# Kernel optimization log

Hardware: AMD Instinct MI355X
Metric: run time of the kernel (lower is better)

The kernel has to match this reference:

```python
import jax, jax.numpy as jnp
import numpy as np

G = 8          # num_groups
GIN = 2048 // G   # group_in_features
GOUT = 2048 // G  # group_out_features


def setup_inputs() -> dict:
    key = jax.random.key(0)
    kx, kw, kb = jax.random.split(key, 3)
    x = jax.random.normal(kx, (8192, 2048), dtype=jnp.float32)
    # per-group linear params, torch nn.Linear default init scale ~ U(-1/sqrt(fan_in), ...)
    bound = 1.0 / np.sqrt(GIN)
    W = jax.random.uniform(kw, (G, GIN, GOUT), minval=-bound, maxval=bound, dtype=jnp.float32)
    b = jax.random.uniform(kb, (G, GOUT), minval=-bound, maxval=bound, dtype=jnp.float32)
    # rational activation coeffs, init p=[1,0,0,0], q=[1,0,0] per group
    p = jnp.tile(jnp.array([1.0, 0.0, 0.0, 0.0], dtype=jnp.float32), (G, 1))
    q = jnp.tile(jnp.array([1.0, 0.0, 0.0], dtype=jnp.float32), (G, 1))
    return {"x": x, "W": W, "b": b, "p": p, "q": q}


def _rational(y, p, q):
    # y: [N, G, GOUT]; p: [G, 4]; q: [G, 3] -> broadcast over N and GOUT
    p = p[None, :, :, None]  # [1,G,4,1]
    q = q[None, :, :, None]  # [1,G,3,1]
    y2 = y * y
    y3 = y2 * y
    num = p[:, :, 0] + p[:, :, 1] * y + p[:, :, 2] * y2 + p[:, :, 3] * y3
    den = 1.0 + jnp.abs(q[:, :, 0] * y + q[:, :, 1] * y2 + q[:, :, 2] * y3)
    return num / den


def reference(x, W, b, p, q):
    N = x.shape[0]
    xg = x.reshape(N, G, GIN)                       # chunk along last dim
    y = jnp.einsum('ngi,gio->ngo', xg, W) + b[None]  # grouped GEMM, [N,G,GOUT]
    out = _rational(y, p, q)
    return out.reshape(N, G * GOUT)                 # cat along last dim
```

## Files before the change

kernel.cpp:

```cpp
#include <hip/hip_runtime.h>
#include <hip/hip_bf16.h>

#define G_ 8
#define GIN_ 256
#define GOUT_ 256
#define NROWS_ 8192
#define LDX_ 2048

typedef __attribute__((ext_vector_type(4))) float f32x4;
typedef __attribute__((ext_vector_type(8))) short bf16x8;

__device__ __forceinline__ void lds_barrier() {
    asm volatile("s_waitcnt lgkmcnt(0)\n\ts_barrier" ::: "memory");
}

__global__ __launch_bounds__(256) void wprep_kernel(const float* __restrict__ W,
                                                    __hip_bfloat16* __restrict__ Wt) {
    __shared__ float tile[64][65];
    const int bid = blockIdx.x;
    const int g  = bid >> 4;
    const int ot = (bid >> 2) & 3;
    const int it = bid & 3;
    const float* Wg = W + g * GIN_ * GOUT_;
    __hip_bfloat16* Wtg = Wt + g * GIN_ * GOUT_;
    const int lane_o = threadIdx.x & 63;
    const int sub    = threadIdx.x >> 6;
#pragma unroll
    for (int r = 0; r < 16; ++r) {
        int i = r * 4 + sub;
        tile[i][lane_o] = Wg[(it * 64 + i) * GOUT_ + ot * 64 + lane_o];
    }
    __syncthreads();
#pragma unroll
    for (int r = 0; r < 16; ++r) {
        int o = r * 4 + sub;
        Wtg[(ot * 64 + o) * GIN_ + it * 64 + lane_o] = __float2bfloat16(tile[lane_o][o]);
    }
}

__global__ __launch_bounds__(256, 4) void gkan_kernel(const float* __restrict__ x,
                                                      const __hip_bfloat16* __restrict__ Wt,
                                                      const float* __restrict__ bias,
                                                      const float* __restrict__ pc,
                                                      const float* __restrict__ qc,
                                                      float* __restrict__ out) {
    __shared__ __align__(16) __hip_bfloat16 As[32 * 256];

    const int bid    = blockIdx.x;
    const int g      = bid & 7;
    const int ch     = (bid >> 3) & 1;
    const int mblock = bid >> 4;
    const int row0   = mblock * 32;

    const int t    = threadIdx.x;
    const int wave = t >> 6;
    const int lane = t & 63;
    const int lm   = lane & 15;
    const int quad = lane >> 4;
    const int colbase = ch * 128 + wave * 32;

    const int sr = t >> 3;
    const int su = t & 7;
    const float* xs = x + (size_t)(row0 + sr) * LDX_ + g * GIN_ + su * 32;
    f32x4 st[8];
#pragma unroll
    for (int j = 0; j < 8; ++j)
        st[j] = *(const f32x4*)(xs + j * 4);

    bf16x8 Breg[2][8];
    {
        const __hip_bfloat16* Wg = Wt + (size_t)g * (GIN_ * GOUT_)
                                      + (size_t)colbase * GIN_;
#pragma unroll
        for (int nt = 0; nt < 2; ++nt)
#pragma unroll
            for (int c = 0; c < 8; ++c)
                Breg[nt][c] = *(const bf16x8*)(Wg + (size_t)(nt * 16 + lm) * GIN_
                                                  + c * 32 + quad * 8);
    }

    const float p0 = pc[g * 4 + 0], p1 = pc[g * 4 + 1];
    const float p2 = pc[g * 4 + 2], p3 = pc[g * 4 + 3];
    const float q0 = qc[g * 3 + 0], q1 = qc[g * 3 + 1], q2 = qc[g * 3 + 2];
    float bb[2];
#pragma unroll
    for (int nt = 0; nt < 2; ++nt)
        bb[nt] = bias[g * GOUT_ + colbase + nt * 16 + lm];

    {
        __hip_bfloat16* rowp = &As[sr * 256];
#pragma unroll
        for (int k = 0; k < 4; ++k) {
            union { __hip_bfloat16 h[8]; bf16x8 v; } cv;
            const f32x4 a = st[2 * k], b = st[2 * k + 1];
            cv.h[0] = __float2bfloat16(a.x); cv.h[1] = __float2bfloat16(a.y);
            cv.h[2] = __float2bfloat16(a.z); cv.h[3] = __float2bfloat16(a.w);
            cv.h[4] = __float2bfloat16(b.x); cv.h[5] = __float2bfloat16(b.y);
            cv.h[6] = __float2bfloat16(b.z); cv.h[7] = __float2bfloat16(b.w);
            *(bf16x8*)(rowp + (((4 * su + k) ^ (sr & 7)) * 8)) = cv.v;
        }
    }
    lds_barrier();

    f32x4 acc[2][2] = {};
#pragma unroll
    for (int c = 0; c < 8; ++c) {
        bf16x8 af[2];
#pragma unroll
        for (int mt = 0; mt < 2; ++mt) {
            const int gh = (c * 4 + quad) ^ (lm & 7);
            af[mt] = *(const bf16x8*)(As + (mt * 16 + lm) * 256 + gh * 8);
        }
#pragma unroll
        for (int mt = 0; mt < 2; ++mt)
#pragma unroll
            for (int nt = 0; nt < 2; ++nt)
                acc[mt][nt] = __builtin_amdgcn_mfma_f32_16x16x32_bf16(
                    af[mt], Breg[nt][c], acc[mt][nt], 0, 0, 0);
    }

#pragma unroll
    for (int nt = 0; nt < 2; ++nt) {
        const int col = g * GOUT_ + colbase + nt * 16 + lm;
#pragma unroll
        for (int mt = 0; mt < 2; ++mt)
#pragma unroll
            for (int r = 0; r < 4; ++r) {
                const int row = row0 + mt * 16 + quad * 4 + r;
                const float y   = acc[mt][nt][r] + bb[nt];
                const float num = p0 + y * (p1 + y * (p2 + y * p3));
                const float den = 1.0f + fabsf(y * (q0 + y * (q1 + y * q2)));
                out[(size_t)row * LDX_ + col] = num * __builtin_amdgcn_rcpf(den);
            }
    }
}

extern "C" void kernel_launch(void* const* d_in, const int* in_sizes, int n_in,
                              void* d_out, int out_size, void* d_ws, size_t ws_size,
                              hipStream_t stream) {
    const float* x = (const float*)d_in[0];
    const float* W = (const float*)d_in[1];
    const float* b = (const float*)d_in[2];
    const float* p = (const float*)d_in[3];
    const float* q = (const float*)d_in[4];
    float* out = (float*)d_out;

    __hip_bfloat16* Wt = (__hip_bfloat16*)d_ws;

    wprep_kernel<<<128, 256, 0, stream>>>(W, Wt);
    gkan_kernel<<<4096, 256, 0, stream>>>(x, Wt, b, p, q, out);
}
```

Baseline: 150.8 us.

## Pre-tile weights into MFMA fragment order and widen block to full group

The weight prep kernel now writes bf16 weights directly in MFMA fragment layout, so each lane loads its B fragment with one contiguous 16-byte read per k-step. The main kernel uses 512-thread blocks covering all 256 output columns of a group, which halves the grid and removes the duplicate x-tile load and conversion that two column halves previously did. B fragments are streamed inside a non-unrolled k loop instead of being preloaded into registers, and the A tile uses a new blocked, swizzled LDS layout. This lowers register pressure and x traffic, at the cost of global weight loads sitting on the MFMA critical path with less latency hiding.

Measured after the change: 133.3 us. -11.6%, faster.

```diff
diff --git a/kernel.cpp b/kernel.cpp
--- a/kernel.cpp
+++ b/kernel.cpp
@@ -19,64 +19,97 @@
     __shared__ float tile[64][65];
     const int bid = blockIdx.x;
     const int g  = bid >> 4;
-    const int ot = (bid >> 2) & 3;
-    const int it = bid & 3;
-    const float* Wg = W + g * GIN_ * GOUT_;
-    __hip_bfloat16* Wtg = Wt + g * GIN_ * GOUT_;
+    const int kt = (bid >> 2) & 3;
+    const int ct = bid & 3;
+    const float* Wg = W + g * (GIN_ * GOUT_);
+    __hip_bfloat16* Wo = Wt + (size_t)g * (GIN_ * GOUT_);
     const int lane_o = threadIdx.x & 63;
     const int sub    = threadIdx.x >> 6;
 #pragma unroll
     for (int r = 0; r < 16; ++r) {
         int i = r * 4 + sub;
-        tile[i][lane_o] = Wg[(it * 64 + i) * GOUT_ + ot * 64 + lane_o];
+        tile[i][lane_o] = Wg[(kt * 64 + i) * GOUT_ + ct * 64 + lane_o];
     }
     __syncthreads();
+    const int col = threadIdx.x & 63;
+    const int kgb = threadIdx.x >> 6;
 #pragma unroll
-    for (int r = 0; r < 16; ++r) {
-        int o = r * 4 + sub;
-        Wtg[(ot * 64 + o) * GIN_ + it * 64 + lane_o] = __float2bfloat16(tile[lane_o][o]);
+    for (int h = 0; h < 2; ++h) {
+        const int kg    = kgb + h * 4;
+        const int kglob = kt * 64 + kg * 8;
+        const int c     = kglob >> 5;
+        const int quad  = (kglob >> 3) & 3;
+        const int colg  = ct * 64 + col;
+        const int cb    = colg >> 4;
+        const int c16   = colg & 15;
+        union { __hip_bfloat16 hh[8]; bf16x8 v; } cv;
+#pragma unroll
+        for (int j = 0; j < 8; ++j)
+            cv.hh[j] = __float2bfloat16(tile[kg * 8 + j][col]);
+        *(bf16x8*)(Wo + (size_t)(c * 16 + cb) * 512 + c16 * 32 + quad * 8) = cv.v;
     }
 }
 
-__global__ __launch_bounds__(256, 4) void gkan_kernel(const float* __restrict__ x,
+__global__ __launch_bounds__(512, 8) void gkan_kernel(const float* __restrict__ x,
                                                       const __hip_bfloat16* __restrict__ Wt,
                                                       const float* __restrict__ bias,
                                                       const float* __restrict__ pc,
                                                       const float* __restrict__ qc,
                                                       float* __restrict__ out) {
-    __shared__ __align__(16) __hip_bfloat16 As[32 * 256];
+    __shared__ __align__(16) __hip_bfloat16 As[8192];
 
-    const int bid    = blockIdx.x;
-    const int g      = bid & 7;
-    const int ch     = (bid >> 3) & 1;
-    const int mblock = bid >> 4;
-    const int row0   = mblock * 32;
+    const int bid  = blockIdx.x;
+    const int g    = bid & 7;
+    const int row0 = (bid >> 3) * 32;
 
     const int t    = threadIdx.x;
     const int wave = t >> 6;
     const int lane = t & 63;
     const int lm   = lane & 15;
-    const int quad = lane >> 4;
-    const int colbase = ch * 128 + wave * 32;
+    const int q    = lane >> 4;
 
-    const int sr = t >> 3;
-    const int su = t & 7;
-    const float* xs = x + (size_t)(row0 + sr) * LDX_ + g * GIN_ + su * 32;
-    f32x4 st[8];
-#pragma unroll
-    for (int j = 0; j < 8; ++j)
-        st[j] = *(const f32x4*)(xs + j * 4);
+    const int row = t >> 4;
+    const int su  = t & 15;
+    const float* xs = x + (size_t)(row0 + row) * LDX_ + g * GIN_ + su * 8;
+    f32x4 a0 = *(const f32x4*)(xs);
+    f32x4 a1 = *(const f32x4*)(xs + 4);
+    f32x4 b0 = *(const f32x4*)(xs + 128);
+    f32x4 b1 = *(const f32x4*)(xs + 132);
 
-    bf16x8 Breg[2][8];
     {
-        const __hip_bfloat16* Wg = Wt + (size_t)g * (GIN_ * GOUT_)
-                                      + (size_t)colbase * GIN_;
-#pragma unroll
-        for (int nt = 0; nt < 2; ++nt)
-#pragma unroll
-            for (int c = 0; c < 8; ++c)
-                Breg[nt][c] = *(const bf16x8*)(Wg + (size_t)(nt * 16 + lm) * GIN_
-                                                  + c * 32 + quad * 8);
+        const int rblk = row >> 4, r16 = row & 15, rx = row & 3;
+        const int c0 = su >> 2, quad = su & 3;
+        const int slot = (quad ^ rx) * 8 + r16 * 32;
+        union { __hip_bfloat16 hh[8]; bf16x8 v; } ca, cb;
+        ca.hh[0] = __float2bfloat16(a0.x); ca.hh[1] = __float2bfloat16(a0.y);
+        ca.hh[2] = __float2bfloat16(a0.z); ca.hh[3] = __float2bfloat16(a0.w);
+        ca.hh[4] = __float2bfloat16(a1.x); ca.hh[5] = __float2bfloat16(a1.y);
+        ca.hh[6] = __float2bfloat16(a1.z); ca.hh[7] = __float2bfloat16(a1.w);
+        cb.hh[0] = __float2bfloat16(b0.x); cb.hh[1] = __float2bfloat16(b0.y);
+        cb.hh[2] = __float2bfloat16(b0.z); cb.hh[3] = __float2bfloat16(b0.w);
+        cb.hh[4] = __float2bfloat16(b1.x); cb.hh[5] = __float2bfloat16(b1.y);
+        cb.hh[6] = __float2bfloat16(b1.z); cb.hh[7] = __float2bfloat16(b1.w);
+        *(bf16x8*)(As + (c0 * 2 + rblk) * 512 + slot)       = ca.v;
+        *(bf16x8*)(As + ((4 + c0) * 2 + rblk) * 512 + slot) = cb.v;
+    }
+    lds_barrier();
+
+    f32x4 acc[2][2] = {};
+    const __hip_bfloat16* bp = Wt + (size_t)g * (GIN_ * GOUT_)
+                                  + (wave * 2) * 512 + lm * 32 + q * 8;
+    const __hip_bfloat16* ap = As + lm * 32 + ((q ^ (lm & 3)) * 8);
+#pragma unroll 1
+    for (int c = 0; c < 8; ++c) {
+        const bf16x8 bf0 = *(const bf16x8*)(bp);
+        const bf16x8 bf1 = *(const bf16x8*)(bp + 512);
+        const bf16x8 af0 = *(const bf16x8*)(ap);
+        const bf16x8 af1 = *(const bf16x8*)(ap + 512);
+        acc[0][0] = __builtin_amdgcn_mfma_f32_16x16x32_bf16(af0, bf0, acc[0][0], 0, 0, 0);
+        acc[0][1] = __builtin_amdgcn_mfma_f32_16x16x32_bf16(af0, bf1, acc[0][1], 0, 0, 0);
+        acc[1][0] = __builtin_amdgcn_mfma_f32_16x16x32_bf16(af1, bf0, acc[1][0], 0, 0, 0);
+        acc[1][1] = __builtin_amdgcn_mfma_f32_16x16x32_bf16(af1, bf1, acc[1][1], 0, 0, 0);
+        bp += 16 * 512;
+        ap += 2 * 512;
     }
 
     const float p0 = pc[g * 4 + 0], p1 = pc[g * 4 + 1];
@@ -85,52 +118,20 @@
     float bb[2];
 #pragma unroll
     for (int nt = 0; nt < 2; ++nt)
-        bb[nt] = bias[g * GOUT_ + colbase + nt * 16 + lm];
-
-    {
-        __hip_bfloat16* rowp = &As[sr * 256];
-#pragma unroll
-        for (int k = 0; k < 4; ++k) {
-            union { __hip_bfloat16 h[8]; bf16x8 v; } cv;
-            const f32x4 a = st[2 * k], b = st[2 * k + 1];
-            cv.h[0] = __float2bfloat16(a.x); cv.h[1] = __float2bfloat16(a.y);
-            cv.h[2] = __float2bfloat16(a.z); cv.h[3] = __float2bfloat16(a.w);
-            cv.h[4] = __float2bfloat16(b.x); cv.h[5] = __float2bfloat16(b.y);
-            cv.h[6] = __float2bfloat16(b.z); cv.h[7] = __float2bfloat16(b.w);
-            *(bf16x8*)(rowp + (((4 * su + k) ^ (sr & 7)) * 8)) = cv.v;
-        }
-    }
-    lds_barrier();
-
-    f32x4 acc[2][2] = {};
-#pragma unroll
-    for (int c = 0; c < 8; ++c) {
-        bf16x8 af[2];
-#pragma unroll
-        for (int mt = 0; mt < 2; ++mt) {
-            const int gh = (c * 4 + quad) ^ (lm & 7);
-            af[mt] = *(const bf16x8*)(As + (mt * 16 + lm) * 256 + gh * 8);
-        }
-#pragma unroll
-        for (int mt = 0; mt < 2; ++mt)
-#pragma unroll
-            for (int nt = 0; nt < 2; ++nt)
-                acc[mt][nt] = __builtin_amdgcn_mfma_f32_16x16x32_bf16(
-                    af[mt], Breg[nt][c], acc[mt][nt], 0, 0, 0);
-    }
+        bb[nt] = bias[g * GOUT_ + wave * 32 + nt * 16 + lm];
 
 #pragma unroll
     for (int nt = 0; nt < 2; ++nt) {
-        const int col = g * GOUT_ + colbase + nt * 16 + lm;
+        const int col = g * GOUT_ + wave * 32 + nt * 16 + lm;
 #pragma unroll
         for (int mt = 0; mt < 2; ++mt)
 #pragma unroll
             for (int r = 0; r < 4; ++r) {
-                const int row = row0 + mt * 16 + quad * 4 + r;
+                const int row_o = row0 + mt * 16 + q * 4 + r;
                 const float y   = acc[mt][nt][r] + bb[nt];
                 const float num = p0 + y * (p1 + y * (p2 + y * p3));
                 const float den = 1.0f + fabsf(y * (q0 + y * (q1 + y * q2)));
-                out[(size_t)row * LDX_ + col] = num * __builtin_amdgcn_rcpf(den);
+                out[(size_t)row_o * LDX_ + col] = num * __builtin_amdgcn_rcpf(den);
             }
     }
 }
@@ -148,5 +149,5 @@
     __hip_bfloat16* Wt = (__hip_bfloat16*)d_ws;
 
     wprep_kernel<<<128, 256, 0, stream>>>(W, Wt);
-    gkan_kernel<<<4096, 256, 0, stream>>>(x, Wt, b, p, q, out);
+    gkan_kernel<<<2048, 512, 0, stream>>>(x, Wt, b, p, q, out);
 }
```
